# Performance work log

Measured on AMD Instinct MI355X. Metric: run time of the kernel, lower is better.

The kernel has to match this reference:

```python
import jax, jax.numpy as jnp
import numpy as np
import math

DIM = 256
B, S = 4, 2048


def setup_inputs() -> dict:
    key = jax.random.key(0)
    ks = jax.random.split(key, 8)
    h = DIM // 2
    return {
        "features": jax.random.normal(ks[0], (B, S, DIM), dtype=jnp.float32),
        "W1": jax.random.normal(ks[1], (DIM, h), dtype=jnp.float32) / np.sqrt(DIM),
        "b1": jnp.zeros((h,), dtype=jnp.float32),
        "ln_g": jnp.ones((h,), dtype=jnp.float32),
        "ln_b": jnp.zeros((h,), dtype=jnp.float32),
        "W2": jax.random.normal(ks[2], (h, 1), dtype=jnp.float32) / np.sqrt(h),
        "b2": jnp.zeros((1,), dtype=jnp.float32),
        "target_entropy": jnp.full((1,), math.log(DIM), dtype=jnp.float32),
        "temperature": jnp.ones((1,), dtype=jnp.float32),
    }


def _compute_entropy(features, temperature):
    b, s, d = features.shape
    x = features.reshape(-1, d)  # [N, D]
    sq = jnp.sum(x * x, axis=-1)  # [N]
    # squared euclidean distance (cdist(...)**2), clamped for numerical safety
    d2 = jnp.maximum(sq[:, None] + sq[None, :] - 2.0 * (x @ x.T), 0.0)  # [N, N]
    kernel = jnp.exp(-d2 / (2.0 * temperature[0] ** 2))
    probs = kernel / jnp.sum(kernel, axis=-1, keepdims=True)
    entropy = -jnp.sum(probs * jnp.log(probs + 1e-6), axis=-1)
    return entropy.reshape(b, s)


def _entropy_estimator(features, W1, b1, ln_g, ln_b, W2, b2):
    h = features @ W1 + b1  # [B, S, D/2]
    mu = jnp.mean(h, axis=-1, keepdims=True)
    var = jnp.mean((h - mu) ** 2, axis=-1, keepdims=True)
    hn = (h - mu) / jnp.sqrt(var + 1e-5) * ln_g + ln_b
    hg = jax.nn.gelu(hn, approximate=False)
    return (hg @ W2 + b2).squeeze(-1)  # [B, S]


def reference(features, W1, b1, ln_g, ln_b, W2, b2, target_entropy, temperature):
    current_entropy = _compute_entropy(features, temperature)  # [B, S]
    # estimated_entropy is computed in the original forward but unused in outputs
    _est = _entropy_estimator(features, W1, b1, ln_g, ln_b, W2, b2)
    entropy_diff = current_entropy - target_entropy[0]
    control_signal = jax.nn.sigmoid(-entropy_diff / temperature[0])  # [B, S]
    controlled_features = features * control_signal[..., None]
    return controlled_features, control_signal
```

## Files before the change

kernel.cpp:

```cpp
#include <hip/hip_runtime.h>

#define N 8192
#define D 256

typedef short short8 __attribute__((ext_vector_type(8)));
typedef float f32x4 __attribute__((ext_vector_type(4)));

__device__ __forceinline__ unsigned short f2bf(float f) {
    unsigned int u = __float_as_uint(f);
    u += 0x7fffu + ((u >> 16) & 1u);
    return (unsigned short)(u >> 16);
}
__device__ __forceinline__ float bf2f(unsigned short h) {
    return __uint_as_float(((unsigned int)h) << 16);
}

#define GLDS16(g, l) __builtin_amdgcn_global_load_lds(                      \
    (const __attribute__((address_space(1))) void*)(g),                     \
    (__attribute__((address_space(3))) void*)(l), 16, 0, 0)

__global__ __launch_bounds__(256) void k_cvt(const float* __restrict__ x,
                                             unsigned short* __restrict__ xb,
                                             float* __restrict__ sq,
                                             float* __restrict__ Sarr,
                                             float* __restrict__ Larr) {
    const int wv = threadIdx.x >> 6, lane = threadIdx.x & 63;
    const int row = blockIdx.x * 4 + wv;
    const float4 v = ((const float4*)x)[(size_t)row * 64 + lane];
    unsigned short pa = f2bf(v.x), pb = f2bf(v.y), pc = f2bf(v.z), pd = f2bf(v.w);
    float a = bf2f(pa), b = bf2f(pb), c = bf2f(pc), d = bf2f(pd);
    float s = a * a + b * b + c * c + d * d;
    ((ushort4*)xb)[(size_t)row * 64 + lane] = make_ushort4(pa, pb, pc, pd);
#pragma unroll
    for (int m = 1; m < 64; m <<= 1) s += __shfl_xor(s, m, 64);
    if (lane == 0) {
        sq[row] = s;
        Sarr[row] = 0.0f;
        Larr[row] = 0.0f;
    }
}

__global__ __launch_bounds__(256, 2) void k_gram(const unsigned short* __restrict__ xb,
                                                 const float* __restrict__ sq,
                                                 const float* __restrict__ temp,
                                                 float* __restrict__ Sarr,
                                                 float* __restrict__ Larr) {
    __shared__ unsigned short Bs[2][64 * D];

    const int tid = threadIdx.x;
    const int wv = tid >> 6, lane = tid & 63;
    const int q8 = lane >> 4, c = lane & 15;
    const int rowbase = blockIdx.x * 256;
    const int ybase = blockIdx.y * 512;
    const float T = temp[0];
    const float LOG2E = 1.44269504f;
    const float s2 = -LOG2E / (2.0f * T * T);
    const float c2 = -2.0f * s2;

    short8 av[4][8];
#pragma unroll
    for (int tr = 0; tr < 4; ++tr) {
        const unsigned short* ap = xb + (size_t)(rowbase + wv * 64 + tr * 16 + c) * D;
#pragma unroll
        for (int kk = 0; kk < 8; ++kk)
            av[tr][kk] = *(const short8*)(ap + kk * 32 + q8 * 8);
    }
    float ar[16];
#pragma unroll
    for (int tr = 0; tr < 4; ++tr)
#pragma unroll
        for (int r = 0; r < 4; ++r)
            ar[tr * 4 + r] = sq[rowbase + wv * 64 + tr * 16 + q8 * 4 + r] * s2;
    float armax = ar[0];
#pragma unroll
    for (int k = 1; k < 16; ++k) armax = fmaxf(armax, ar[k]);

    float Sr[16], Mr[16];
#pragma unroll
    for (int k = 0; k < 16; ++k) { Sr[k] = 0.f; Mr[k] = 0.f; }

#pragma unroll
    for (int g2 = 0; g2 < 8; ++g2) {
        int s = wv * 8 + g2;
        const unsigned short* src =
            xb + (size_t)(ybase + ((s >> 3) << 4) + c) * D + ((s & 7) << 5) + (q8 << 3);
        GLDS16(src, &Bs[0][0] + s * 512);
    }

    for (int ht = 0; ht < 8; ++ht) {
        const int tilebase = ybase + ht * 64;
        const int cur = ht & 1;

        __syncthreads();

        if (ht < 7) {
            const int nb = tilebase + 64;
#pragma unroll
            for (int g2 = 0; g2 < 8; ++g2) {
                int s = wv * 8 + g2;
                const unsigned short* src =
                    xb + (size_t)(nb + ((s >> 3) << 4) + c) * D + ((s & 7) << 5) + (q8 << 3);
                GLDS16(src, &Bs[cur ^ 1][0] + s * 512);
            }
        }

#pragma unroll
        for (int tc = 0; tc < 4; ++tc) {
            const float bc = sq[tilebase + tc * 16 + c] * s2;
            const unsigned short* bb = &Bs[cur][0] + tc * 8 * 512 + lane * 8;

            short8 bva[4];
#pragma unroll
            for (int kk = 0; kk < 4; ++kk)
                bva[kk] = *(const short8*)(bb + kk * 512);

            f32x4 acc[4];
#pragma unroll
            for (int tr = 0; tr < 4; ++tr)
#pragma unroll
                for (int r = 0; r < 4; ++r) acc[tr][r] = 0.0f;

#pragma unroll
            for (int kk = 0; kk < 4; ++kk)
#pragma unroll
                for (int tr = 0; tr < 4; ++tr)
                    acc[tr] = __builtin_amdgcn_mfma_f32_16x16x32_bf16(
                        av[tr][kk], bva[kk], acc[tr], 0, 0, 0);

            short8 bvb[4];
#pragma unroll
            for (int kk = 0; kk < 4; ++kk)
                bvb[kk] = *(const short8*)(bb + (kk + 4) * 512);

#pragma unroll
            for (int kk = 0; kk < 4; ++kk)
#pragma unroll
                for (int tr = 0; tr < 4; ++tr)
                    acc[tr] = __builtin_amdgcn_mfma_f32_16x16x32_bf16(
                        av[tr][kk + 4], bvb[kk], acc[tr], 0, 0, 0);

            float gmax = acc[0][0];
#pragma unroll
            for (int tr = 0; tr < 4; ++tr)
#pragma unroll
                for (int r = 0; r < 4; ++r) gmax = fmaxf(gmax, acc[tr][r]);
            const float bound = fmaf(gmax, c2, armax + bc);

            if (__any(bound >= -115.0f)) {
#pragma unroll
                for (int tr = 0; tr < 4; ++tr)
#pragma unroll
                    for (int r = 0; r < 4; ++r) {
                        float g = acc[tr][r];
                        float t2 = fminf(fmaf(g, c2, ar[tr * 4 + r] + bc), 0.0f);
                        float e = __builtin_amdgcn_exp2f(t2);
                        Sr[tr * 4 + r] += e;
                        Mr[tr * 4 + r] = fmaf(e, t2, Mr[tr * 4 + r]);
                    }
            }
        }
    }

#pragma unroll
    for (int m = 1; m <= 8; m <<= 1)
#pragma unroll
        for (int k = 0; k < 16; ++k) {
            Sr[k] += __shfl_xor(Sr[k], m, 64);
            Mr[k] += __shfl_xor(Mr[k], m, 64);
        }
    if (c == 0) {
        const float LN2 = 0.69314718f;
#pragma unroll
        for (int k = 0; k < 16; ++k) {
            int row = rowbase + wv * 64 + (k >> 2) * 16 + q8 * 4 + (k & 3);
            atomicAdd(&Sarr[row], Sr[k]);
            atomicAdd(&Larr[row], Mr[k] * LN2);
        }
    }
}

__global__ __launch_bounds__(256) void k_finish(const float* __restrict__ x,
                                                const float* __restrict__ Sarr,
                                                const float* __restrict__ Larr,
                                                const float* __restrict__ target,
                                                const float* __restrict__ temp,
                                                float* __restrict__ out) {
    const int gid = blockIdx.x * 256 + threadIdx.x;
    const int row = gid >> 6;
    float S = Sarr[row], L = Larr[row];
    float H = __logf(S) - L / S;
    float z = (H - target[0]) / temp[0];
    float cs = 1.0f / (1.0f + __expf(z));
    float4 v = ((const float4*)x)[gid];
    float4 o;
    o.x = v.x * cs; o.y = v.y * cs; o.z = v.z * cs; o.w = v.w * cs;
    ((float4*)out)[gid] = o;
    if ((gid & 63) == 0) out[(size_t)N * D + row] = cs;
}

extern "C" void kernel_launch(void* const* d_in, const int* in_sizes, int n_in,
                              void* d_out, int out_size, void* d_ws, size_t ws_size,
                              hipStream_t stream) {
    const float* x = (const float*)d_in[0];
    const float* target = (const float*)d_in[7];
    const float* temp = (const float*)d_in[8];
    float* out = (float*)d_out;

    float* wsf = (float*)d_ws;
    float* sq = wsf;
    float* Sarr = wsf + N;
    float* Larr = wsf + 2 * N;

    const size_t need = 3 * (size_t)N * sizeof(float) + (size_t)N * D * sizeof(unsigned short);
    unsigned short* xb = (ws_size >= need) ? (unsigned short*)(wsf + 3 * N)
                                           : (unsigned short*)d_out;

    k_cvt<<<N / 4, 256, 0, stream>>>(x, xb, sq, Sarr, Larr);
    k_gram<<<dim3(32, 16), 256, 0, stream>>>(xb, sq, temp, Sarr, Larr);
    k_finish<<<(N * (D / 4)) / 256, 256, 0, stream>>>(x, Sarr, Larr, target, temp, out);
}
```

Baseline: 122.4 us.

## Store bf16 features in MFMA-fragment-swizzled layout for contiguous loads

The conversion kernel now writes the bf16 copy of the features in a layout grouped by 16-row blocks and K-chunks, matching the per-lane MFMA operand order. The gram kernel's A-register loads and global-to-LDS B-tile loads then read fully contiguous 1 KB chunks instead of strided row segments, which should improve coalescing. The conversion kernel now handles 16 rows per wave with strided float4 reads, so its own access pattern is less coalesced.

```diff
diff --git a/kernel.cpp b/kernel.cpp
--- a/kernel.cpp
+++ b/kernel.cpp
@@ -20,27 +20,42 @@
     (__attribute__((address_space(3))) void*)(l), 16, 0, 0)
 
 __global__ __launch_bounds__(256) void k_cvt(const float* __restrict__ x,
-                                             unsigned short* __restrict__ xb,
+                                             unsigned short* __restrict__ xb2,
                                              float* __restrict__ sq,
                                              float* __restrict__ Sarr,
                                              float* __restrict__ Larr) {
     const int wv = threadIdx.x >> 6, lane = threadIdx.x & 63;
-    const int row = blockIdx.x * 4 + wv;
-    const float4 v = ((const float4*)x)[(size_t)row * 64 + lane];
-    unsigned short pa = f2bf(v.x), pb = f2bf(v.y), pc = f2bf(v.z), pd = f2bf(v.w);
-    float a = bf2f(pa), b = bf2f(pb), c = bf2f(pc), d = bf2f(pd);
-    float s = a * a + b * b + c * c + d * d;
-    ((ushort4*)xb)[(size_t)row * 64 + lane] = make_ushort4(pa, pb, pc, pd);
-#pragma unroll
-    for (int m = 1; m < 64; m <<= 1) s += __shfl_xor(s, m, 64);
-    if (lane == 0) {
-        sq[row] = s;
+    const int c = lane & 15, q8 = lane >> 4;
+    const int grp = blockIdx.x * 4 + wv;
+    const int row = grp * 16 + c;
+
+    float ssum = 0.0f;
+#pragma unroll
+    for (int kk = 0; kk < 8; ++kk) {
+        const float4* gp = (const float4*)(x + (size_t)row * D + kk * 32 + q8 * 8);
+        float4 v0 = gp[0], v1 = gp[1];
+        unsigned short h[8];
+        h[0] = f2bf(v0.x); h[1] = f2bf(v0.y); h[2] = f2bf(v0.z); h[3] = f2bf(v0.w);
+        h[4] = f2bf(v1.x); h[5] = f2bf(v1.y); h[6] = f2bf(v1.z); h[7] = f2bf(v1.w);
+        short8 p;
+#pragma unroll
+        for (int i = 0; i < 8; ++i) {
+            float f = bf2f(h[i]);
+            ssum = fmaf(f, f, ssum);
+            p[i] = (short)h[i];
+        }
+        ((short8*)xb2)[(grp * 8 + kk) * 64 + lane] = p;
+    }
+    ssum += __shfl_xor(ssum, 16, 64);
+    ssum += __shfl_xor(ssum, 32, 64);
+    if (q8 == 0) {
+        sq[row] = ssum;
         Sarr[row] = 0.0f;
         Larr[row] = 0.0f;
     }
 }
 
-__global__ __launch_bounds__(256, 2) void k_gram(const unsigned short* __restrict__ xb,
+__global__ __launch_bounds__(256, 2) void k_gram(const unsigned short* __restrict__ xb2,
                                                  const float* __restrict__ sq,
                                                  const float* __restrict__ temp,
                                                  float* __restrict__ Sarr,
@@ -60,10 +75,10 @@
     short8 av[4][8];
 #pragma unroll
     for (int tr = 0; tr < 4; ++tr) {
-        const unsigned short* ap = xb + (size_t)(rowbase + wv * 64 + tr * 16 + c) * D;
+        const int grp = (rowbase >> 4) + wv * 4 + tr;
 #pragma unroll
         for (int kk = 0; kk < 8; ++kk)
-            av[tr][kk] = *(const short8*)(ap + kk * 32 + q8 * 8);
+            av[tr][kk] = ((const short8*)xb2)[(grp * 8 + kk) * 64 + lane];
     }
     float ar[16];
 #pragma unroll
@@ -82,8 +97,7 @@
 #pragma unroll
     for (int g2 = 0; g2 < 8; ++g2) {
         int s = wv * 8 + g2;
-        const unsigned short* src =
-            xb + (size_t)(ybase + ((s >> 3) << 4) + c) * D + ((s & 7) << 5) + (q8 << 3);
+        const unsigned short* src = xb2 + (size_t)(ybase >> 4) * 4096 + s * 512 + lane * 8;
         GLDS16(src, &Bs[0][0] + s * 512);
     }
 
@@ -94,12 +108,11 @@
         __syncthreads();
 
         if (ht < 7) {
-            const int nb = tilebase + 64;
+            const size_t nchunk = (size_t)((tilebase + 64) >> 4) * 4096;
 #pragma unroll
             for (int g2 = 0; g2 < 8; ++g2) {
                 int s = wv * 8 + g2;
-                const unsigned short* src =
-                    xb + (size_t)(nb + ((s >> 3) << 4) + c) * D + ((s & 7) << 5) + (q8 << 3);
+                const unsigned short* src = xb2 + nchunk + s * 512 + lane * 8;
                 GLDS16(src, &Bs[cur ^ 1][0] + s * 512);
             }
         }
@@ -212,10 +225,10 @@
     float* Larr = wsf + 2 * N;
 
     const size_t need = 3 * (size_t)N * sizeof(float) + (size_t)N * D * sizeof(unsigned short);
-    unsigned short* xb = (ws_size >= need) ? (unsigned short*)(wsf + 3 * N)
-                                           : (unsigned short*)d_out;
-
-    k_cvt<<<N / 4, 256, 0, stream>>>(x, xb, sq, Sarr, Larr);
-    k_gram<<<dim3(32, 16), 256, 0, stream>>>(xb, sq, temp, Sarr, Larr);
+    unsigned short* xb2 = (ws_size >= need) ? (unsigned short*)(wsf + 3 * N)
+                                            : (unsigned short*)d_out;
+
+    k_cvt<<<N / 64, 256, 0, stream>>>(x, xb2, sq, Sarr, Larr);
+    k_gram<<<dim3(32, 16), 256, 0, stream>>>(xb2, sq, temp, Sarr, Larr);
     k_finish<<<(N * (D / 4)) / 256, 256, 0, stream>>>(x, Sarr, Larr, target, temp, out);
 }
```

Measured after the change: 113.3 us. -7.5%, faster.
